# Performance work log

Hardware: AMD Instinct MI355X
Metric: run time of the kernel (lower is better)

Reference implementation:

```python
import jax, jax.numpy as jnp
import numpy as np

D_MODEL = 768
MLP_DIM = 3072
N_EXPERTS = 8
TOP_K = 2
GROUP_DET = 1024
GROUP_CLS = 128


def _route(x, wr, k, capacity):
    """Deterministic top-k softmax router with capacity (vmoe-style).

    x: [G, S, d], wr: [d, E]. Returns dispatch [G,S,E,C] (0/1) and
    combine [G,S,E,C] (gate-weighted).
    """
    G, S, _ = x.shape
    E = wr.shape[1]
    gates = jax.nn.softmax(jnp.einsum('gsd,de->gse', x, wr))  # [G,S,E]
    gval, gidx = jax.lax.top_k(gates, k)                      # [G,S,k]
    # rank-major ordering: all rank-0 choices first, then rank-1, ...
    idx = jnp.swapaxes(gidx, 1, 2).reshape(G, k * S)          # [G,kS]
    val = jnp.swapaxes(gval, 1, 2).reshape(G, k * S)
    oh = jax.nn.one_hot(idx, E, dtype=x.dtype)                # [G,kS,E]
    # position of each assignment in its expert's buffer
    pos = jnp.take_along_axis(jnp.cumsum(oh, axis=1), idx[..., None], axis=2)[..., 0] - 1.0
    keep = (pos < capacity).astype(x.dtype)                   # drop overflow tokens
    posc = jnp.where(pos < capacity, pos, 0.0).astype(jnp.int32)
    slot = jax.nn.one_hot(posc, capacity, dtype=x.dtype)      # [G,kS,C]
    disp = oh[:, :, :, None] * slot[:, :, None, :] * keep[:, :, None, None]  # [G,kS,E,C]
    disp = disp.reshape(G, k, S, E, capacity)
    combine = (disp * val.reshape(G, k, S, 1, 1)).sum(axis=1)  # [G,S,E,C]
    dispatch = disp.sum(axis=1)                                # [G,S,E,C]
    return dispatch, combine


def _expert_mlp(xe, w1, b1, w2, b2):
    # xe: [E,G,C,d]; per-expert params w1:[E,d,m], b1:[E,m], w2:[E,m,d], b2:[E,d]
    h = jax.nn.gelu(jnp.einsum('egcd,edm->egcm', xe, w1) + b1[:, None, None, :])
    return jnp.einsum('egcm,emd->egcd', h, w2) + b2[:, None, None, :]


def _moe_stream(x3, group_size, wr, w1, b1, w2, b2):
    B, S, d = x3.shape
    x = x3.reshape(-1, group_size, d)                         # [G,gs,d]
    capacity = group_size * TOP_K // N_EXPERTS
    dispatch, combine = _route(x, wr, TOP_K, capacity)
    xe = jnp.einsum('gsec,gsd->egcd', dispatch, x)            # gather to experts
    ye = _expert_mlp(xe, w1, b1, w2, b2)                      # grouped MLP
    y = jnp.einsum('gsec,egcd->gsd', combine, ye)             # weighted scatter back
    return y.reshape(B, S, d)


def setup_inputs() -> dict:
    key = jax.random.key(0)
    ks = jax.random.split(key, 8)
    xav1 = float(np.sqrt(6.0 / (D_MODEL + MLP_DIM)))
    xavr = float(np.sqrt(6.0 / (D_MODEL + N_EXPERTS)))
    return {
        'inputs_det': jax.random.normal(ks[0], (8, 1024, D_MODEL), jnp.float32),
        'inputs_cls': jax.random.normal(ks[1], (8, 128, D_MODEL), jnp.float32),
        'wr_det': jax.random.uniform(ks[2], (D_MODEL, N_EXPERTS), jnp.float32, -xavr, xavr),
        'wr_cls': jax.random.uniform(ks[3], (D_MODEL, N_EXPERTS), jnp.float32, -xavr, xavr),
        'w1': jax.random.uniform(ks[4], (N_EXPERTS, D_MODEL, MLP_DIM), jnp.float32, -xav1, xav1),
        'b1': jax.random.normal(ks[5], (N_EXPERTS, MLP_DIM), jnp.float32) * 1e-6,
        'w2': jax.random.uniform(ks[6], (N_EXPERTS, MLP_DIM, D_MODEL), jnp.float32, -xav1, xav1),
        'b2': jax.random.normal(ks[7], (N_EXPERTS, D_MODEL), jnp.float32) * 1e-6,
    }


def reference(inputs_det, inputs_cls, wr_det, wr_cls, w1, b1, w2, b2):
    out_det = _moe_stream(inputs_det, GROUP_DET, wr_det, w1, b1, w2, b2)
    out_cls = _moe_stream(inputs_cls, GROUP_CLS, wr_cls, w1, b1, w2, b2)
    return (out_det, out_cls)
```

## Files before the change

### kernel.cpp

```cpp
#include <hip/hip_runtime.h>
#include <hip/hip_bf16.h>
#include <math.h>

typedef __bf16 bf16;
typedef __bf16 bf16x8 __attribute__((ext_vector_type(8)));
typedef __bf16 bf16x4 __attribute__((ext_vector_type(4)));
typedef float  f32x4  __attribute__((ext_vector_type(4)));

#define D_MODEL 768
#define MLP_DIM 3072

#define SZ_W1T   ((size_t)8*3072*768*2)
#define SZ_W2T   ((size_t)8*768*3072*2)
#define SZ_XED   ((size_t)8*8*256*768*2)
#define SZ_XEC   ((size_t)8*8*32*768*2)
#define SZ_HD    ((size_t)8*2048*3072*2)
#define SZ_HC    ((size_t)8*256*3072*2)
#define SZ_YED   ((size_t)8*2048*768*2)
#define SZ_YEC   ((size_t)8*256*768*2)
#define SZ_RID   ((size_t)8192*8)
#define SZ_RGD   ((size_t)8192*8)
#define SZ_RIC   ((size_t)1024*8)
#define SZ_RGC   ((size_t)1024*8)
#define SZ_STD   ((size_t)8*8*256*4)
#define SZ_STC   ((size_t)8*8*32*4)
#define SZ_TSD   ((size_t)2*8192*4)
#define SZ_TSC   ((size_t)2*1024*4)

#define OFF_W1T  ((size_t)0)
#define OFF_W2T  (OFF_W1T + SZ_W1T)
#define OFF_XED  (OFF_W2T + SZ_W2T)
#define OFF_XEC  (OFF_XED + SZ_XED)
#define OFF_HD   (OFF_XEC + SZ_XEC)
#define OFF_HC   (OFF_HD  + SZ_HD)
#define OFF_YED  (OFF_HC  + SZ_HC)
#define OFF_YEC  (OFF_YED + SZ_YED)
#define OFF_RID  (OFF_YEC + SZ_YEC)
#define OFF_RGD  (OFF_RID + SZ_RID)
#define OFF_RIC  (OFF_RGD + SZ_RGD)
#define OFF_RGC  (OFF_RIC + SZ_RIC)
#define OFF_STD  (OFF_RGC + SZ_RGC)
#define OFF_STC  (OFF_STD + SZ_STD)
#define OFF_TSD  (OFF_STC + SZ_STC)
#define OFF_TSC  (OFF_TSD + SZ_TSD)

__device__ __forceinline__ void lds_load16(const void* g, void* l) {
  __builtin_amdgcn_global_load_lds((__attribute__((address_space(1))) void*)g,
                                   (__attribute__((address_space(3))) void*)l,
                                   16, 0, 0);
}

__device__ __forceinline__ float gelu_fast(float x) {
  float x2 = x * x;
  float z = x * __builtin_fmaf(-0.07135481627f, x2, -1.5957691216f);
  float e = __expf(z);
  return x * __builtin_amdgcn_rcpf(1.f + e);
}

__global__ void convt_router_kernel(const float* __restrict__ w1, bf16* __restrict__ w1t,
                                    const float* __restrict__ w2, bf16* __restrict__ w2t,
                                    const float* __restrict__ xd, const float* __restrict__ wrd,
                                    const float* __restrict__ xc, const float* __restrict__ wrc,
                                    int2* __restrict__ rid, float2* __restrict__ rgd,
                                    int2* __restrict__ ric, float2* __restrict__ rgc) {
  int bid = blockIdx.x;
  if (bid < 2304) {
    const float *x, *wr; int2* ridx; float2* rgate;
    if (bid < 2048) { x = xd; wr = wrd; ridx = rid; rgate = rgd; }
    else { bid -= 2048; x = xc; wr = wrc; ridx = ric; rgate = rgc; }
    int wave = threadIdx.x >> 6;
    int lane = threadIdx.x & 63;
    int t = bid * 4 + wave;
    const float* xr = x + (size_t)t * D_MODEL;
    float acc[8];
#pragma unroll
    for (int e = 0; e < 8; ++e) acc[e] = 0.f;
    for (int d = lane; d < D_MODEL; d += 64) {
      float xv = xr[d];
      const float* w = wr + d * 8;
      float4 a = *(const float4*)w;
      float4 b = *(const float4*)(w + 4);
      acc[0] += xv * a.x; acc[1] += xv * a.y; acc[2] += xv * a.z; acc[3] += xv * a.w;
      acc[4] += xv * b.x; acc[5] += xv * b.y; acc[6] += xv * b.z; acc[7] += xv * b.w;
    }
#pragma unroll
    for (int off = 32; off > 0; off >>= 1) {
#pragma unroll
      for (int e = 0; e < 8; ++e) acc[e] += __shfl_xor(acc[e], off, 64);
    }
    float mx = acc[0];
#pragma unroll
    for (int e = 1; e < 8; ++e) mx = fmaxf(mx, acc[e]);
    float p[8]; float z = 0.f;
#pragma unroll
    for (int e = 0; e < 8; ++e) { p[e] = __expf(acc[e] - mx); z += p[e]; }
    int i1 = 0;
#pragma unroll
    for (int e = 1; e < 8; ++e) if (p[e] > p[i1]) i1 = e;
    int i2 = (i1 == 0) ? 1 : 0;
#pragma unroll
    for (int e = 0; e < 8; ++e) if (e != i1 && p[e] > p[i2]) i2 = e;
    if (lane == 0) {
      float inv = 1.f / z;
      ridx[t]  = make_int2(i1, i2);
      rgate[t] = make_float2(p[i1] * inv, p[i2] * inv);
    }
    return;
  }
  bid -= 2304;
  __shared__ float tile[64][65];
  const float* src; bf16* dst; int K, N;
  if (bid < 4608) { src = w1; dst = w1t; K = 768; N = 3072; }
  else { bid -= 4608; src = w2; dst = w2t; K = 3072; N = 768; }
  int e = bid / 576;
  int t = bid - e * 576;
  int tiles_x = N >> 6;
  int ky = t / tiles_x;
  int n0 = (t - ky * tiles_x) * 64, k0 = ky * 64;
  const float* S_ = src + (size_t)e * K * N;
  bf16* D_ = dst + (size_t)e * K * N;
  int tx = threadIdx.x & 15, ty = threadIdx.x >> 4;
#pragma unroll
  for (int i = 0; i < 4; ++i) {
    float4 v = *(const float4*)(S_ + (size_t)(k0 + ty + i * 16) * N + (n0 + tx * 4));
    int r = ty + i * 16, c = tx * 4;
    tile[r][c] = v.x; tile[r][c + 1] = v.y; tile[r][c + 2] = v.z; tile[r][c + 3] = v.w;
  }
  __syncthreads();
  int n = threadIdx.x >> 2, kq = (threadIdx.x & 3) * 16;
  bf16 o[16];
#pragma unroll
  for (int j = 0; j < 16; ++j) o[j] = (bf16)tile[kq + j][n];
  bf16* drow = D_ + (size_t)(n0 + n) * K + (k0 + kq);
  *(bf16x8*)drow       = *(const bf16x8*)o;
  *(bf16x8*)(drow + 8) = *(const bf16x8*)(o + 8);
}

__global__ void positions_kernel(const int2* __restrict__ rid, int* __restrict__ std_,
                                 int* __restrict__ tsd_, const int2* __restrict__ ric,
                                 int* __restrict__ stc_, int* __restrict__ tsc_) {
  __shared__ int2 sh[1024];
  int bid = blockIdx.x;
  const int2* ridx; int *slot_token, *tok_slot; int S, C, g;
  if (bid < 8) { ridx = rid; slot_token = std_; tok_slot = tsd_; S = 1024; C = 256; g = bid; }
  else { ridx = ric; slot_token = stc_; tok_slot = tsc_; S = 128; C = 32; g = bid - 8; }
  int lane = threadIdx.x;
  int ntok = 8 * S;
  for (int i = lane; i < S; i += 64) sh[i] = ridx[g * S + i];
  __builtin_amdgcn_s_waitcnt(0);
  unsigned long long ltmask = (1ull << lane) - 1ull;
  int cnt[8];
#pragma unroll
  for (int e = 0; e < 8; ++e) cnt[e] = 0;
  int nch = (2 * S) >> 6;
  for (int ch = 0; ch < nch; ++ch) {
    int a = (ch << 6) + lane;
    int r = (a >= S) ? 1 : 0;
    int s = a - r * S;
    int2 id = sh[s];
    int  e  = r ? id.y : id.x;
    unsigned long long mymask = 0;
    int add[8];
#pragma unroll
    for (int ee = 0; ee < 8; ++ee) {
      unsigned long long mk = __ballot(e == ee);
      if (e == ee) mymask = mk;
      add[ee] = __popcll(mk);
    }
    int pos = cnt[e] + __popcll(mymask & ltmask);
    int sl = (e * 8 + g) * C + pos;
    if (pos < C) slot_token[sl] = s;
    tok_slot[r * ntok + g * S + s] = (pos < C) ? sl : -1;
#pragma unroll
    for (int ee = 0; ee < 8; ++ee) cnt[ee] += add[ee];
  }
#pragma unroll
  for (int e = 0; e < 8; ++e) {
    for (int i = cnt[e] + lane; i < C; i += 64)
      slot_token[(e * 8 + g) * C + i] = -1;
  }
}

__global__ void gather_kernel(const float* __restrict__ xd, const int* __restrict__ std_,
                              bf16* __restrict__ xed, const float* __restrict__ xc,
                              const int* __restrict__ stc_, bf16* __restrict__ xec,
                              int splitd) {
  int bid = blockIdx.x;
  const float* x; const int* slot_token; bf16* xe; int S, C;
  if (bid < splitd) { x = xd; slot_token = std_; xe = xed; S = 1024; C = 256; }
  else { bid -= splitd; x = xc; slot_token = stc_; xe = xec; S = 128; C = 32; }
  int slot = bid * 4 + (threadIdx.x >> 6);
  int lane = threadIdx.x & 63;
  int g = (slot / C) & 7;
  int s = slot_token[slot];
  bf16* dst = xe + (size_t)slot * D_MODEL;
  const float* xr = x + ((size_t)g * S + (s < 0 ? 0 : s)) * D_MODEL;
#pragma unroll
  for (int j = 0; j < 3; ++j) {
    int idx = j * 256 + lane * 4;
    float4 v;
    if (s >= 0) v = *(const float4*)(xr + idx);
    else        v = make_float4(0.f, 0.f, 0.f, 0.f);
    bf16 o[4] = {(bf16)v.x, (bf16)v.y, (bf16)v.z, (bf16)v.w};
    *(uint2*)(dst + idx) = *(const uint2*)o;
  }
}

__global__ void combine_kernel(const int* __restrict__ tsd_, const float2* __restrict__ rgd,
                               const bf16* __restrict__ yed, float* __restrict__ outd,
                               const int* __restrict__ tsc_, const float2* __restrict__ rgc,
                               const bf16* __restrict__ yec, float* __restrict__ outc,
                               int splitd) {
  int bid = blockIdx.x;
  const int* tok_slot; const float2* rgate; const bf16* ye; float* out; int ntok;
  if (bid < splitd) { tok_slot = tsd_; rgate = rgd; ye = yed; out = outd; ntok = 8192; }
  else { bid -= splitd; tok_slot = tsc_; rgate = rgc; ye = yec; out = outc; ntok = 1024; }
  int t = bid * 4 + (threadIdx.x >> 6);
  int lane = threadIdx.x & 63;
  int s1 = tok_slot[t];
  int s2 = tok_slot[ntok + t];
  float2 gg = rgate[t];
  float g1 = (s1 < 0) ? 0.f : gg.x;
  float g2 = (s2 < 0) ? 0.f : gg.y;
  const bf16* y1 = ye + (size_t)(s1 < 0 ? 0 : s1) * D_MODEL;
  const bf16* y2 = ye + (size_t)(s2 < 0 ? 0 : s2) * D_MODEL;
  float* orow = out + (size_t)t * D_MODEL;
#pragma unroll
  for (int j = 0; j < 3; ++j) {
    int idx = j * 256 + lane * 4;
    bf16x4 a = *(const bf16x4*)(y1 + idx);
    bf16x4 b = *(const bf16x4*)(y2 + idx);
    float4 o;
    o.x = g1 * (float)a[0] + g2 * (float)b[0];
    o.y = g1 * (float)a[1] + g2 * (float)b[1];
    o.z = g1 * (float)a[2] + g2 * (float)b[2];
    o.w = g1 * (float)a[3] + g2 * (float)b[3];
    *(float4*)(orow + idx) = o;
  }
}

template <int GELU>
__launch_bounds__(256, 3)
__global__ void gemm_mfma(const bf16* __restrict__ Adet, const bf16* __restrict__ Acls,
                          const bf16* __restrict__ Btall, const float* __restrict__ biasall,
                          int Mdet, int Mcls, int N, int K,
                          int Nmd, int Nmc, int Nn, int minner, int splitd,
                          bf16* __restrict__ Odet, bf16* __restrict__ Ocls) {
  int bid = blockIdx.x;
  const bf16* Aall; bf16* Oall; int M, Nm;
  if (bid < splitd) { Aall = Adet; Oall = Odet; M = Mdet; Nm = Nmd; }
  else { bid -= splitd; Aall = Acls; Oall = Ocls; M = Mcls; Nm = Nmc; }
  const int e   = bid & 7;
  const int seq = bid >> 3;
  int m_t, n_t;
  if (minner) { n_t = seq / Nm; m_t = seq - n_t * Nm; }
  else        { m_t = seq / Nn; n_t = seq - m_t * Nn; }
  const int n0 = n_t * 128;
  const int m0 = m_t * 128;
  const int tid  = threadIdx.x;
  const int wave = tid >> 6, lane = tid & 63;
  const int wm = (wave >> 1) * 64, wn = (wave & 1) * 64;
  const int lrow = lane & 15, lquad = lane >> 4;

  __shared__ __align__(16) bf16 smem[16384];
  bf16* As = smem;
  bf16* Bs = smem + 8192;

  const bf16* A  = Aall  + (size_t)e * M * K;
  const bf16* Bt = Btall + (size_t)e * N * K;

  const int srow = tid >> 3;
  const int gq   = (tid & 7) ^ (srow & 7);
  const bf16* Asrc = A  + (size_t)(m0 + srow) * K + gq * 8;
  const bf16* Bsrc = Bt + (size_t)(n0 + srow) * K + gq * 8;
  char* AsB = (char*)As;
  char* BsB = (char*)Bs;
  const int ldsw = wave * 1024;

  const float* bias = biasall + (size_t)e * N;
  float bfr[4];
#pragma unroll
  for (int ni = 0; ni < 4; ++ni) bfr[ni] = bias[n0 + wn + ni * 16 + lrow];

  f32x4 acc[4][4];
#pragma unroll
  for (int mi = 0; mi < 4; ++mi)
#pragma unroll
    for (int ni = 0; ni < 4; ++ni) acc[mi][ni] = {0.f, 0.f, 0.f, 0.f};

  const int xsw = lrow & 7;
  const int nsteps = K >> 6;
  for (int kt = 0; kt < nsteps; ++kt) {
    const bf16* a0 = Asrc + kt * 64;
    const bf16* b0 = Bsrc + kt * 64;
#pragma unroll
    for (int rd = 0; rd < 4; ++rd) {
      lds_load16(a0 + (size_t)(rd * 32) * K, AsB + rd * 4096 + ldsw);
      lds_load16(b0 + (size_t)(rd * 32) * K, BsB + rd * 4096 + ldsw);
    }
    __syncthreads();
#pragma unroll
    for (int h = 0; h < 2; ++h) {
      bf16x8 fa[4], fb[4];
      const int ca = ((h * 4 + lquad) ^ xsw) * 8;
#pragma unroll
      for (int i = 0; i < 4; ++i) {
        fa[i] = *(const bf16x8*)(As + (wm + i * 16 + lrow) * 64 + ca);
        fb[i] = *(const bf16x8*)(Bs + (wn + i * 16 + lrow) * 64 + ca);
      }
#pragma unroll
      for (int mi = 0; mi < 4; ++mi)
#pragma unroll
        for (int ni = 0; ni < 4; ++ni)
          acc[mi][ni] = __builtin_amdgcn_mfma_f32_16x16x32_bf16(fa[mi], fb[ni], acc[mi][ni], 0, 0, 0);
    }
    __syncthreads();
  }

#pragma unroll
  for (int mi = 0; mi < 4; ++mi) {
#pragma unroll
    for (int r = 0; r < 4; ++r) {
      int row = wm + mi * 16 + lquad * 4 + r;
#pragma unroll
      for (int ni = 0; ni < 4; ++ni) {
        int colL = wn + ni * 16 + lrow;
        float v = acc[mi][ni][r] + bfr[ni];
        if (GELU) v = gelu_fast(v);
        int chunk = (colL >> 3) ^ (row & 7);
        smem[row * 128 + chunk * 8 + (colL & 7)] = (bf16)v;
      }
    }
  }
  __syncthreads();
  bf16* O = Oall + (size_t)e * M * N;
#pragma unroll
  for (int it = 0; it < 8; ++it) {
    int idx = it * 256 + tid;
    int row = idx >> 4;
    int ck  = idx & 15;
    int pchunk = ck ^ (row & 7);
    bf16x8 vv = *(const bf16x8*)(smem + row * 128 + pchunk * 8);
    *(bf16x8*)(O + (size_t)(m0 + row) * N + n0 + ck * 8) = vv;
  }
}

template <int GELU>
__launch_bounds__(512, 2)
__global__ void gemm_mfma8p(const bf16* __restrict__ Adet, const bf16* __restrict__ Acls,
                            const bf16* __restrict__ Btall, const float* __restrict__ biasall,
                            int Mdet, int Mcls, int N, int K,
                            int Nmd, int Nmc, int Nn, int minner, int splitd,
                            bf16* __restrict__ Odet, bf16* __restrict__ Ocls) {
  int bid = blockIdx.x;
  const bf16* Aall; bf16* Oall; int M, Nm;
  if (bid < splitd) { Aall = Adet; Oall = Odet; M = Mdet; Nm = Nmd; }
  else { bid -= splitd; Aall = Acls; Oall = Ocls; M = Mcls; Nm = Nmc; }
  const int e   = bid & 7;
  const int seq = bid >> 3;
  int m_t, n_t;
  if (minner) { n_t = seq / Nm; m_t = seq - n_t * Nm; }
  else        { m_t = seq / Nn; n_t = seq - m_t * Nn; }
  const int n0 = n_t * 256;
  const int m0 = m_t * 256;
  const int tid  = threadIdx.x;
  const int wave = tid >> 6, lane = tid & 63;
  const int wm = (wave >> 2) * 128, wn = (wave & 3) * 64;
  const int lrow = lane & 15, lquad = lane >> 4;

  __shared__ __align__(16) bf16 smem[65536];
  char* smemB = (char*)smem;

  const bf16* A  = Aall  + (size_t)e * M * K;
  const bf16* Bt = Btall + (size_t)e * N * K;

  const int srow0 = tid >> 3;
  const int gq    = (tid & 7) ^ (srow0 & 7);
  const bf16* Asrc = A  + (size_t)(m0 + srow0) * K + gq * 8;
  const bf16* Bsrc = Bt + (size_t)(n0 + srow0) * K + gq * 8;
  const int ldsw = wave * 1024;

  const int aBase = (wm ? 8192 : 0) + lrow * 64;
  const int bBase = 16384 + (wn >= 128 ? 8192 : 0) + (wn & 64) * 64 + lrow * 64;
  const int ca0 = (lquad ^ (lrow & 7)) * 8;
  const int ca1 = ca0 ^ 32;

  const float* bias = biasall + (size_t)e * N;
  float bfr[4];
#pragma unroll
  for (int ni = 0; ni < 4; ++ni) bfr[ni] = bias[n0 + wn + ni * 16 + lrow];

  f32x4 acc[8][4];
#pragma unroll
  for (int mi = 0; mi < 8; ++mi)
#pragma unroll
    for (int ni = 0; ni < 4; ++ni) acc[mi][ni] = {0.f, 0.f, 0.f, 0.f};

  bf16x8 fa[2][4], fb0[2][2], fb1[2][2];

#define STG_A(buf, half, kt) do { \
    const bf16* _s = Asrc + (size_t)((half) * 128) * K + (size_t)(kt) * 64; \
    char* _d = smemB + (buf) * 65536 + (half) * 16384 + ldsw; \
    lds_load16(_s, _d); \
    lds_load16(_s + (size_t)64 * K, _d + 8192); \
  } while (0)
#define STG_B(buf, half, kt) do { \
    const bf16* _s = Bsrc + (size_t)((half) * 128) * K + (size_t)(kt) * 64; \
    char* _d = smemB + (buf) * 65536 + 32768 + (half) * 16384 + ldsw; \
    lds_load16(_s, _d); \
    lds_load16(_s + (size_t)64 * K, _d + 8192); \
  } while (0)
#define LDA(buf, qm) do { \
    const bf16* _p = smem + (buf) * 32768 + aBase + (qm) * 4096; \
    _Pragma("unroll") \
    for (int _i = 0; _i < 4; ++_i) { \
      fa[0][_i] = *(const bf16x8*)(_p + _i * 1024 + ca0); \
      fa[1][_i] = *(const bf16x8*)(_p + _i * 1024 + ca1); \
    } \
  } while (0)
#define LDB(buf, qn, FB) do { \
    const bf16* _p = smem + (buf) * 32768 + bBase + (qn) * 2048; \
    _Pragma("unroll") \
    for (int _j = 0; _j < 2; ++_j) { \
      FB[0][_j] = *(const bf16x8*)(_p + _j * 1024 + ca0); \
      FB[1][_j] = *(const bf16x8*)(_p + _j * 1024 + ca1); \
    } \
  } while (0)
#define MM(qm, qn, FB) do { \
    __builtin_amdgcn_s_setprio(1); \
    _Pragma("unroll") \
    for (int _h = 0; _h < 2; ++_h) \
      _Pragma("unroll") \
      for (int _i = 0; _i < 4; ++_i) \
        _Pragma("unroll") \
        for (int _j = 0; _j < 2; ++_j) \
          acc[(qm) * 4 + _i][(qn) * 2 + _j] = __builtin_amdgcn_mfma_f32_16x16x32_bf16( \
              fa[_h][_i], FB[_h][_j], acc[(qm) * 4 + _i][(qn) * 2 + _j], 0, 0, 0); \
    __builtin_amdgcn_s_setprio(0); \
  } while (0)
#define BAR() __builtin_amdgcn_s_barrier()
#define VMC4() asm volatile("s_waitcnt vmcnt(4)" ::: "memory")

  const int nt = K >> 6;
  const int niter = nt >> 1;

  STG_B(0, 0, 0); STG_B(0, 1, 0); STG_A(0, 0, 0); STG_A(0, 1, 0);
  STG_B(1, 0, 1); STG_B(1, 1, 1);
  VMC4();
  BAR();

  for (int it = 0; it < niter; ++it) {
    const int k1 = 2 * it + 1;
    const int k2 = (2 * it + 2 < nt) ? 2 * it + 2 : nt - 1;
    const int k3 = (2 * it + 3 < nt) ? 2 * it + 3 : nt - 1;
    LDA(0, 0); LDB(0, 0, fb0); STG_A(1, 0, k1); BAR(); MM(0, 0, fb0); BAR();
    LDB(0, 1, fb1);            STG_A(1, 1, k1); BAR(); MM(0, 1, fb1); BAR();
    LDA(0, 1);                 STG_B(0, 0, k2); BAR(); MM(1, 1, fb1); BAR();
                               STG_B(0, 1, k2); VMC4();
                                                BAR(); MM(1, 0, fb0); BAR();
    LDA(1, 0); LDB(1, 0, fb0); STG_A(0, 0, k2); BAR(); MM(0, 0, fb0); BAR();
    LDB(1, 1, fb1);            STG_A(0, 1, k2); BAR(); MM(0, 1, fb1); BAR();
    LDA(1, 1);                 STG_B(1, 0, k3); BAR(); MM(1, 1, fb1); BAR();
                               STG_B(1, 1, k3); VMC4();
                                                BAR(); MM(1, 0, fb0); BAR();
  }

#undef STG_A
#undef STG_B
#undef LDA
#undef LDB
#undef MM
#undef BAR
#undef VMC4

  __syncthreads();
#pragma unroll
  for (int mi = 0; mi < 8; ++mi) {
#pragma unroll
    for (int r = 0; r < 4; ++r) {
      int row = wm + mi * 16 + lquad * 4 + r;
#pragma unroll
      for (int ni = 0; ni < 4; ++ni) {
        int colL = wn + ni * 16 + lrow;
        float v = acc[mi][ni][r] + bfr[ni];
        if (GELU) v = gelu_fast(v);
        int chunk = (colL >> 3) ^ (row & 7);
        smem[row * 256 + chunk * 8 + (colL & 7)] = (bf16)v;
      }
    }
  }
  __syncthreads();
  bf16* O = Oall + (size_t)e * M * N;
#pragma unroll
  for (int itw = 0; itw < 16; ++itw) {
    int idx = itw * 512 + tid;
    int row = idx >> 5;
    int ck  = idx & 31;
    int pchunk = ck ^ (row & 7);
    bf16x8 vv = *(const bf16x8*)(smem + row * 256 + pchunk * 8);
    *(bf16x8*)(O + (size_t)(m0 + row) * N + n0 + ck * 8) = vv;
  }
}

extern "C" void kernel_launch(void* const* d_in, const int* in_sizes, int n_in,
                              void* d_out, int out_size, void* d_ws, size_t ws_size,
                              hipStream_t stream) {
  (void)in_sizes; (void)n_in; (void)ws_size; (void)out_size;
  const float* x_det  = (const float*)d_in[0];
  const float* x_cls  = (const float*)d_in[1];
  const float* wr_det = (const float*)d_in[2];
  const float* wr_cls = (const float*)d_in[3];
  const float* w1     = (const float*)d_in[4];
  const float* b1     = (const float*)d_in[5];
  const float* w2     = (const float*)d_in[6];
  const float* b2     = (const float*)d_in[7];
  float* out = (float*)d_out;
  char*  ws  = (char*)d_ws;

  bf16*   w1t    = (bf16*)(ws + OFF_W1T);
  bf16*   w2t    = (bf16*)(ws + OFF_W2T);
  bf16*   xe_det = (bf16*)(ws + OFF_XED);
  bf16*   xe_cls = (bf16*)(ws + OFF_XEC);
  bf16*   h_det  = (bf16*)(ws + OFF_HD);
  bf16*   h_cls  = (bf16*)(ws + OFF_HC);
  bf16*   ye_det = (bf16*)(ws + OFF_YED);
  bf16*   ye_cls = (bf16*)(ws + OFF_YEC);
  int2*   ri_det = (int2*)(ws + OFF_RID);
  float2* rg_det = (float2*)(ws + OFF_RGD);
  int2*   ri_cls = (int2*)(ws + OFF_RIC);
  float2* rg_cls = (float2*)(ws + OFF_RGC);
  int*    st_det = (int*)(ws + OFF_STD);
  int*    st_cls = (int*)(ws + OFF_STC);
  int*    ts_det = (int*)(ws + OFF_TSD);
  int*    ts_cls = (int*)(ws + OFF_TSC);

  convt_router_kernel<<<2304 + 2 * 4608, 256, 0, stream>>>(
      w1, w1t, w2, w2t, x_det, wr_det, x_cls, wr_cls,
      ri_det, rg_det, ri_cls, rg_cls);

  positions_kernel<<<16, 64, 0, stream>>>(ri_det, st_det, ts_det, ri_cls, st_cls, ts_cls);

  gather_kernel<<<4096 + 512, 256, 0, stream>>>(x_det, st_det, xe_det, x_cls, st_cls, xe_cls, 4096);

  gemm_mfma<1><<<8 * 16 * 24 + 8 * 2 * 24, 256, 0, stream>>>(
      xe_det, xe_cls, w1t, b1, 2048, 256, 3072, 768,
      16, 2, 24, 1, 8 * 16 * 24, h_det, h_cls);

  gemm_mfma8p<0><<<8 * 8 * 3 + 8 * 1 * 3, 512, 0, stream>>>(
      h_det, h_cls, w2t, b2, 2048, 256, 768, 3072,
      8, 1, 3, 0, 8 * 8 * 3, ye_det, ye_cls);

  combine_kernel<<<2048 + 256, 256, 0, stream>>>(ts_det, rg_det, ye_det, out,
                                                 ts_cls, rg_cls, ye_cls,
                                                 out + (size_t)8192 * 768, 2048);
}
```

Baseline: 436.6 us.

## Spread weight transposes across later kernels to overlap with gather and GEMM

Splits the combined convert/router kernel so the router runs alone. The w1 fp32-to-bf16 transpose moves into the gather kernel and the w2 transpose rides as extra tail blocks of the first GEMM launch. The aim is to hide transpose bandwidth behind other work and shorten the critical path before routing. The GEMM kernel now declares its shared buffer before the early-exit branch so the transpose blocks can reuse it.

```diff
diff --git a/kernel.cpp b/kernel.cpp
--- a/kernel.cpp
+++ b/kernel.cpp
@@ -57,83 +57,79 @@
   return x * __builtin_amdgcn_rcpf(1.f + e);
 }
 
-__global__ void convt_router_kernel(const float* __restrict__ w1, bf16* __restrict__ w1t,
-                                    const float* __restrict__ w2, bf16* __restrict__ w2t,
-                                    const float* __restrict__ xd, const float* __restrict__ wrd,
-                                    const float* __restrict__ xc, const float* __restrict__ wrc,
-                                    int2* __restrict__ rid, float2* __restrict__ rgd,
-                                    int2* __restrict__ ric, float2* __restrict__ rgc) {
-  int bid = blockIdx.x;
-  if (bid < 2304) {
-    const float *x, *wr; int2* ridx; float2* rgate;
-    if (bid < 2048) { x = xd; wr = wrd; ridx = rid; rgate = rgd; }
-    else { bid -= 2048; x = xc; wr = wrc; ridx = ric; rgate = rgc; }
-    int wave = threadIdx.x >> 6;
-    int lane = threadIdx.x & 63;
-    int t = bid * 4 + wave;
-    const float* xr = x + (size_t)t * D_MODEL;
-    float acc[8];
-#pragma unroll
-    for (int e = 0; e < 8; ++e) acc[e] = 0.f;
-    for (int d = lane; d < D_MODEL; d += 64) {
-      float xv = xr[d];
-      const float* w = wr + d * 8;
-      float4 a = *(const float4*)w;
-      float4 b = *(const float4*)(w + 4);
-      acc[0] += xv * a.x; acc[1] += xv * a.y; acc[2] += xv * a.z; acc[3] += xv * a.w;
-      acc[4] += xv * b.x; acc[5] += xv * b.y; acc[6] += xv * b.z; acc[7] += xv * b.w;
-    }
-#pragma unroll
-    for (int off = 32; off > 0; off >>= 1) {
-#pragma unroll
-      for (int e = 0; e < 8; ++e) acc[e] += __shfl_xor(acc[e], off, 64);
-    }
-    float mx = acc[0];
-#pragma unroll
-    for (int e = 1; e < 8; ++e) mx = fmaxf(mx, acc[e]);
-    float p[8]; float z = 0.f;
-#pragma unroll
-    for (int e = 0; e < 8; ++e) { p[e] = __expf(acc[e] - mx); z += p[e]; }
-    int i1 = 0;
-#pragma unroll
-    for (int e = 1; e < 8; ++e) if (p[e] > p[i1]) i1 = e;
-    int i2 = (i1 == 0) ? 1 : 0;
-#pragma unroll
-    for (int e = 0; e < 8; ++e) if (e != i1 && p[e] > p[i2]) i2 = e;
-    if (lane == 0) {
-      float inv = 1.f / z;
-      ridx[t]  = make_int2(i1, i2);
-      rgate[t] = make_float2(p[i1] * inv, p[i2] * inv);
-    }
-    return;
-  }
-  bid -= 2304;
-  __shared__ float tile[64][65];
-  const float* src; bf16* dst; int K, N;
-  if (bid < 4608) { src = w1; dst = w1t; K = 768; N = 3072; }
-  else { bid -= 4608; src = w2; dst = w2t; K = 3072; N = 768; }
-  int e = bid / 576;
-  int t = bid - e * 576;
+__device__ __forceinline__ void transpose64(const float* __restrict__ src,
+                                            bf16* __restrict__ dst,
+                                            int K, int N, int e, int t, float* tile) {
   int tiles_x = N >> 6;
   int ky = t / tiles_x;
   int n0 = (t - ky * tiles_x) * 64, k0 = ky * 64;
   const float* S_ = src + (size_t)e * K * N;
   bf16* D_ = dst + (size_t)e * K * N;
-  int tx = threadIdx.x & 15, ty = threadIdx.x >> 4;
+  int tid = threadIdx.x;
+  int tx = tid & 15, ty = tid >> 4;
 #pragma unroll
   for (int i = 0; i < 4; ++i) {
     float4 v = *(const float4*)(S_ + (size_t)(k0 + ty + i * 16) * N + (n0 + tx * 4));
     int r = ty + i * 16, c = tx * 4;
-    tile[r][c] = v.x; tile[r][c + 1] = v.y; tile[r][c + 2] = v.z; tile[r][c + 3] = v.w;
+    tile[r * 65 + c] = v.x; tile[r * 65 + c + 1] = v.y;
+    tile[r * 65 + c + 2] = v.z; tile[r * 65 + c + 3] = v.w;
   }
   __syncthreads();
-  int n = threadIdx.x >> 2, kq = (threadIdx.x & 3) * 16;
+  int n = tid >> 2, kq = (tid & 3) * 16;
   bf16 o[16];
 #pragma unroll
-  for (int j = 0; j < 16; ++j) o[j] = (bf16)tile[kq + j][n];
+  for (int j = 0; j < 16; ++j) o[j] = (bf16)tile[(kq + j) * 65 + n];
   bf16* drow = D_ + (size_t)(n0 + n) * K + (k0 + kq);
   *(bf16x8*)drow       = *(const bf16x8*)o;
   *(bf16x8*)(drow + 8) = *(const bf16x8*)(o + 8);
+}
+
+__global__ void router_kernel(const float* __restrict__ xd, const float* __restrict__ wrd,
+                              const float* __restrict__ xc, const float* __restrict__ wrc,
+                              int2* __restrict__ rid, float2* __restrict__ rgd,
+                              int2* __restrict__ ric, float2* __restrict__ rgc,
+                              int splitd) {
+  int bid = blockIdx.x;
+  const float *x, *wr; int2* ridx; float2* rgate;
+  if (bid < splitd) { x = xd; wr = wrd; ridx = rid; rgate = rgd; }
+  else { bid -= splitd; x = xc; wr = wrc; ridx = ric; rgate = rgc; }
+  int wave = threadIdx.x >> 6;
+  int lane = threadIdx.x & 63;
+  int t = bid * 4 + wave;
+  const float* xr = x + (size_t)t * D_MODEL;
+  float acc[8];
+#pragma unroll
+  for (int e = 0; e < 8; ++e) acc[e] = 0.f;
+  for (int d = lane; d < D_MODEL; d += 64) {
+    float xv = xr[d];
+    const float* w = wr + d * 8;
+    float4 a = *(const float4*)w;
+    float4 b = *(const float4*)(w + 4);
+    acc[0] += xv * a.x; acc[1] += xv * a.y; acc[2] += xv * a.z; acc[3] += xv * a.w;
+    acc[4] += xv * b.x; acc[5] += xv * b.y; acc[6] += xv * b.z; acc[7] += xv * b.w;
+  }
+#pragma unroll
+  for (int off = 32; off > 0; off >>= 1) {
+#pragma unroll
+    for (int e = 0; e < 8; ++e) acc[e] += __shfl_xor(acc[e], off, 64);
+  }
+  float mx = acc[0];
+#pragma unroll
+  for (int e = 1; e < 8; ++e) mx = fmaxf(mx, acc[e]);
+  float p[8]; float z = 0.f;
+#pragma unroll
+  for (int e = 0; e < 8; ++e) { p[e] = __expf(acc[e] - mx); z += p[e]; }
+  int i1 = 0;
+#pragma unroll
+  for (int e = 1; e < 8; ++e) if (p[e] > p[i1]) i1 = e;
+  int i2 = (i1 == 0) ? 1 : 0;
+#pragma unroll
+  for (int e = 0; e < 8; ++e) if (e != i1 && p[e] > p[i2]) i2 = e;
+  if (lane == 0) {
+    float inv = 1.f / z;
+    ridx[t]  = make_int2(i1, i2);
+    rgate[t] = make_float2(p[i1] * inv, p[i2] * inv);
+  }
 }
 
 __global__ void positions_kernel(const int2* __restrict__ rid, int* __restrict__ std_,
@@ -181,11 +177,20 @@
   }
 }
 
-__global__ void gather_kernel(const float* __restrict__ xd, const int* __restrict__ std_,
-                              bf16* __restrict__ xed, const float* __restrict__ xc,
-                              const int* __restrict__ stc_, bf16* __restrict__ xec,
-                              int splitd) {
+__global__ void gather_w1t_kernel(const float* __restrict__ xd, const int* __restrict__ std_,
+                                  bf16* __restrict__ xed, const float* __restrict__ xc,
+                                  const int* __restrict__ stc_, bf16* __restrict__ xec,
+                                  int splitd, const float* __restrict__ w1,
+                                  bf16* __restrict__ w1t, int nT) {
+  __shared__ float tile[64 * 65];
   int bid = blockIdx.x;
+  if (bid < nT) {
+    int e = bid / 576;
+    int t = bid - e * 576;
+    transpose64(w1, w1t, 768, 3072, e, t, tile);
+    return;
+  }
+  bid -= nT;
   const float* x; const int* slot_token; bf16* xe; int S, C;
   if (bid < splitd) { x = xd; slot_token = std_; xe = xed; S = 1024; C = 256; }
   else { bid -= splitd; x = xc; slot_token = stc_; xe = xec; S = 128; C = 32; }
@@ -245,8 +250,20 @@
                           const bf16* __restrict__ Btall, const float* __restrict__ biasall,
                           int Mdet, int Mcls, int N, int K,
                           int Nmd, int Nmc, int Nn, int minner, int splitd,
-                          bf16* __restrict__ Odet, bf16* __restrict__ Ocls) {
+                          bf16* __restrict__ Odet, bf16* __restrict__ Ocls,
+                          const float* __restrict__ tsrc, bf16* __restrict__ tdst,
+                          int nGemm) {
+  __shared__ __align__(16) bf16 smem[16384];
+
   int bid = blockIdx.x;
+  if (bid >= nGemm) {
+    int t2 = bid - nGemm;
+    int e = t2 / 576;
+    int t = t2 - e * 576;
+    transpose64(tsrc, tdst, 3072, 768, e, t, (float*)smem);
+    return;
+  }
+
   const bf16* Aall; bf16* Oall; int M, Nm;
   if (bid < splitd) { Aall = Adet; Oall = Odet; M = Mdet; Nm = Nmd; }
   else { bid -= splitd; Aall = Acls; Oall = Ocls; M = Mcls; Nm = Nmc; }
@@ -262,7 +279,6 @@
   const int wm = (wave >> 1) * 64, wn = (wave & 1) * 64;
   const int lrow = lane & 15, lquad = lane >> 4;
 
-  __shared__ __align__(16) bf16 smem[16384];
   bf16* As = smem;
   bf16* Bs = smem + 8192;
 
@@ -534,17 +550,17 @@
   int*    ts_det = (int*)(ws + OFF_TSD);
   int*    ts_cls = (int*)(ws + OFF_TSC);
 
-  convt_router_kernel<<<2304 + 2 * 4608, 256, 0, stream>>>(
-      w1, w1t, w2, w2t, x_det, wr_det, x_cls, wr_cls,
-      ri_det, rg_det, ri_cls, rg_cls);
+  router_kernel<<<2048 + 256, 256, 0, stream>>>(x_det, wr_det, x_cls, wr_cls,
+                                                ri_det, rg_det, ri_cls, rg_cls, 2048);
 
   positions_kernel<<<16, 64, 0, stream>>>(ri_det, st_det, ts_det, ri_cls, st_cls, ts_cls);
 
-  gather_kernel<<<4096 + 512, 256, 0, stream>>>(x_det, st_det, xe_det, x_cls, st_cls, xe_cls, 4096);
-
-  gemm_mfma<1><<<8 * 16 * 24 + 8 * 2 * 24, 256, 0, stream>>>(
+  gather_w1t_kernel<<<4608 + 4096 + 512, 256, 0, stream>>>(
+      x_det, st_det, xe_det, x_cls, st_cls, xe_cls, 4096, w1, w1t, 4608);
+
+  gemm_mfma<1><<<8 * 16 * 24 + 8 * 2 * 24 + 4608, 256, 0, stream>>>(
       xe_det, xe_cls, w1t, b1, 2048, 256, 3072, 768,
-      16, 2, 24, 1, 8 * 16 * 24, h_det, h_cls);
+      16, 2, 24, 1, 8 * 16 * 24, h_det, h_cls, w2, w2t, 3456);
 
   gemm_mfma8p<0><<<8 * 8 * 3 + 8 * 1 * 3, 512, 0, stream>>>(
       h_det, h_cls, w2t, b2, 2048, 256, 768, 3072,
```

After: 421.2 us. 1.04x faster.
